# Kernel tuning notes

Measured on AMD Instinct MI355X. Metric: run time of the kernel, lower is better.

Reference implementation:

```python
import jax, jax.numpy as jnp
import numpy as np

D_MODEL = 1024
N_HEADS = 16
D_HIDDEN = 4096
EPS = 1e-6
MASK_VAL = 1e10


def layernorm(x, gamma, beta):
    # Matches torch module: unbiased std (N-1), divide by (std + eps)
    mean = jnp.mean(x, axis=-1, keepdims=True)
    d = x.shape[-1]
    std = jnp.sqrt(jnp.sum((x - mean) ** 2, axis=-1, keepdims=True) / (d - 1))
    return gamma * (x - mean) / (std + EPS) + beta


def multihead(q_in, k_in, v_in, wq, wk, wv, wo, causal):
    # nn.Linear(bias=False): y = x @ W.T
    q = q_in @ wq.T
    k = k_in @ wk.T
    v = v_in @ wv.T
    B, Sq, D = q.shape
    Sk = k.shape[1]
    H, dh = N_HEADS, D // N_HEADS
    q = q.reshape(B, Sq, H, dh)
    k = k.reshape(B, Sk, H, dh)
    v = v.reshape(B, Sk, H, dh)
    scores = jnp.einsum('bqhd,bkhd->bhqk', q, k)  # [B,H,Sq,Sk]
    if causal:
        tri = jnp.triu(jnp.full((Sk, Sk), MASK_VAL, dtype=scores.dtype), k=1)
        scores = scores - tri  # mask applied BEFORE scaling, as in source
    scale = jnp.sqrt(jnp.asarray(D_MODEL, dtype=scores.dtype))  # d_key = d_model
    att = jax.nn.softmax(scores / scale, axis=-1)
    out = jnp.einsum('bhqk,bkhd->bqhd', att, v).reshape(B, Sq, D)
    return out @ wo.T


def setup_inputs() -> dict:
    key = jax.random.key(0)
    ks = jax.random.split(key, 24)
    B, S, D, DH = 2, 2048, D_MODEL, D_HIDDEN
    w = lambda k, shp: (jax.random.normal(k, shp, dtype=jnp.float32) * 0.02)
    inp = {
        'x': jax.random.normal(ks[0], (B, S, D), dtype=jnp.float32),
        'encoding': jax.random.normal(ks[1], (B, S, D), dtype=jnp.float32),
        'sa_wq': w(ks[2], (D, D)), 'sa_wk': w(ks[3], (D, D)),
        'sa_wv': w(ks[4], (D, D)), 'sa_wo': w(ks[5], (D, D)),
        'ca_wq': w(ks[6], (D, D)), 'ca_wk': w(ks[7], (D, D)),
        'ca_wv': w(ks[8], (D, D)), 'ca_wo': w(ks[9], (D, D)),
        'ff_w1': w(ks[10], (DH, D)), 'ff_b1': jnp.zeros((DH,), jnp.float32),
        'ff_w2': w(ks[11], (D, DH)), 'ff_b2': jnp.zeros((D,), jnp.float32),
        'ln1_g': jnp.ones((D,), jnp.float32), 'ln1_b': jnp.zeros((D,), jnp.float32),
        'ln2_g': jnp.ones((D,), jnp.float32), 'ln2_b': jnp.zeros((D,), jnp.float32),
        'ln3_g': jnp.ones((D,), jnp.float32), 'ln3_b': jnp.zeros((D,), jnp.float32),
    }
    return inp


def reference(x, encoding, sa_wq, sa_wk, sa_wv, sa_wo, ca_wq, ca_wk, ca_wv, ca_wo,
              ff_w1, ff_b1, ff_w2, ff_b2, ln1_g, ln1_b, ln2_g, ln2_b, ln3_g, ln3_b):
    # self-attention (causal) + post-norm residual
    h = layernorm(x + multihead(x, x, x, sa_wq, sa_wk, sa_wv, sa_wo, causal=True), ln1_g, ln1_b)
    # cross-attention + post-norm residual
    h = layernorm(h + multihead(h, encoding, encoding, ca_wq, ca_wk, ca_wv, ca_wo, causal=False), ln2_g, ln2_b)
    # feed-forward + post-norm residual
    ff = jax.nn.relu(h @ ff_w1.T + ff_b1) @ ff_w2.T + ff_b2
    return layernorm(h + ff, ln3_g, ln3_b)
```

## Files before the change

kernel.cpp:

```cpp
#include <hip/hip_runtime.h>
#include <hip/hip_bf16.h>
#include <math.h>

#define D_MODEL 1024
#define NHEADS  16
#define DHEAD   64
#define D_HID   4096

typedef __attribute__((ext_vector_type(8))) short short8;
typedef __attribute__((ext_vector_type(4))) short short4v;
typedef __attribute__((ext_vector_type(4))) float f32x4;
typedef __attribute__((ext_vector_type(16))) float f32x16;
typedef __attribute__((ext_vector_type(2))) unsigned uint2v;

#define QSCALE_F 0.04508422002778011f
#define MASK_T   4.5084220e8f

__device__ inline short f2bs(float x) {
    union { __hip_bfloat16 b; short s; } u;
    u.b = __float2bfloat16(x);
    return u.s;
}
__device__ inline float bs2f(ushort s) {
    union { unsigned u; float f; } v; v.u = ((unsigned)s) << 16; return v.f;
}
__device__ inline unsigned cvtpk(float lo, float hi) {
    unsigned r;
    asm("v_cvt_pk_bf16_f32 %0, %1, %2" : "=v"(r) : "v"(lo), "v"(hi));
    return r;
}
__device__ inline short8 pack8(float4 x, float4 y) {
    short8 v;
    v[0] = f2bs(x.x); v[1] = f2bs(x.y); v[2] = f2bs(x.z); v[3] = f2bs(x.w);
    v[4] = f2bs(y.x); v[5] = f2bs(y.y); v[6] = f2bs(y.z); v[7] = f2bs(y.w);
    return v;
}
typedef const unsigned __attribute__((address_space(1))) gu32;
typedef unsigned __attribute__((address_space(3))) lu32;
__device__ inline void gload16(const void* g, void* l) {
    __builtin_amdgcn_global_load_lds((gu32*)g, (lu32*)l, 16, 0, 0);
}
__device__ inline int swz(int r, int byteInRow) {
    return (r * 128 + byteInRow) ^ ((r & 7) << 4);
}

struct WP { const float* p[10]; };
__global__ __launch_bounds__(256) void cast_weights(WP wp, short* __restrict__ dst) {
    const int n8 = (16 << 20) / 8;
    for (int i = blockIdx.x * 256 + threadIdx.x; i < n8; i += gridDim.x * 256) {
        size_t e = (size_t)i * 8;
        int seg = (int)(e >> 20);
        const float* src;
        if (seg < 8)       src = wp.p[seg] + (e & ((1u << 20) - 1));
        else if (seg < 12) src = wp.p[8] + (e - ((size_t)8 << 20));
        else               src = wp.p[9] + (e - ((size_t)12 << 20));
        float4 a = *(const float4*)src;
        float4 b = *(const float4*)(src + 4);
        *(short8*)(dst + e) = pack8(a, b);
    }
}

__global__ __launch_bounds__(256) void cast_f2b(const float* __restrict__ in,
                                                short* __restrict__ out, int n8) {
    for (int i = blockIdx.x * 256 + threadIdx.x; i < n8; i += gridDim.x * 256) {
        float4 a = *(const float4*)(in + (size_t)i * 8);
        float4 b = *(const float4*)(in + (size_t)i * 8 + 4);
        *(short8*)(out + (size_t)i * 8) = pack8(a, b);
    }
}

template<int OM, bool BIAS, bool RELU, bool ACCUM>
__global__ __launch_bounds__(512) void gemm_mfma(
    const short* __restrict__ A, int lda,
    const short* __restrict__ Bm, int ldb,
    const float* __restrict__ bias,
    float* __restrict__ Cf, short* __restrict__ Cb, int ldc,
    int M, int N, int K, size_t routeElems, float qscale)
{
    __shared__ short Als[2][128 * 64];
    __shared__ short Bls[2][128 * 64];

    const int tid = threadIdx.x, w = tid >> 6, l = tid & 63;
    const int l15 = l & 15, lhi = l >> 4;
    const int wr = w >> 2, wc = w & 3;

    const int kh = (OM == 3) ? blockIdx.z : 0;
    if (OM == 3) {
        A  += (size_t)kh * K;
        Bm += (size_t)kh * K;
    }

    const unsigned nwg  = gridDim.x * gridDim.y;
    const unsigned wgid = blockIdx.y * gridDim.x + blockIdx.x;
    const unsigned cpx  = nwg >> 3;
    const unsigned sid  = (wgid & 7) * cpx + (wgid >> 3);
    const int bm = (int)(sid / gridDim.x) * 128;
    const int bn = (int)(sid % gridDim.x) * 128;

    const int srow = w * 8 + (l >> 3);
    const int schk = ((l & 7) ^ (l >> 3)) * 8;

    f32x4 acc[4][2] = {};

    #pragma unroll
    for (int i = 0; i < 2; ++i) {
        const short* ga = A  + (size_t)(bm + i * 64 + srow) * lda + schk;
        const short* gb = Bm + (size_t)(bn + i * 64 + srow) * ldb + schk;
        gload16(ga, &Als[0][i * 4096 + w * 512 + l * 8]);
        gload16(gb, &Bls[0][i * 4096 + w * 512 + l * 8]);
    }
    __syncthreads();

    const int nIter = K >> 6;
    int cur = 0;
    for (int it = 0; it < nIter; ++it) {
        if (it + 1 < nIter) {
            const int k1 = (it + 1) << 6;
            #pragma unroll
            for (int i = 0; i < 2; ++i) {
                const short* ga = A  + (size_t)(bm + i * 64 + srow) * lda + k1 + schk;
                const short* gb = Bm + (size_t)(bn + i * 64 + srow) * ldb + k1 + schk;
                gload16(ga, &Als[cur ^ 1][i * 4096 + w * 512 + l * 8]);
                gload16(gb, &Bls[cur ^ 1][i * 4096 + w * 512 + l * 8]);
            }
        }

        short8 af[4][2], bf[2][2];
        #pragma unroll
        for (int m = 0; m < 4; ++m) {
            const int row = wr * 64 + m * 16 + l15;
            #pragma unroll
            for (int kk = 0; kk < 2; ++kk)
                af[m][kk] = *(const short8*)&Als[cur][row * 64 + (((kk * 4 + lhi) ^ (l15 & 7)) * 8)];
        }
        #pragma unroll
        for (int n = 0; n < 2; ++n) {
            const int row = wc * 32 + n * 16 + l15;
            #pragma unroll
            for (int kk = 0; kk < 2; ++kk)
                bf[n][kk] = *(const short8*)&Bls[cur][row * 64 + (((kk * 4 + lhi) ^ (l15 & 7)) * 8)];
        }
        __builtin_amdgcn_s_setprio(1);
        #pragma unroll
        for (int kk = 0; kk < 2; ++kk)
            #pragma unroll
            for (int m = 0; m < 4; ++m)
                #pragma unroll
                for (int n = 0; n < 2; ++n)
                    acc[m][n] = __builtin_amdgcn_mfma_f32_16x16x32_bf16(af[m][kk], bf[n][kk], acc[m][n], 0, 0, 0);
        __builtin_amdgcn_s_setprio(0);

        __syncthreads();
        cur ^= 1;
    }

    #pragma unroll
    for (int n = 0; n < 2; ++n) {
        const int col = bn + wc * 32 + n * 16 + l15;
        float bv = 0.f;
        if (BIAS && (OM != 3 || kh == 0)) bv = bias[col];
        const float sc = (OM == 2) ? (col < 1024 ? qscale : 1.f) : qscale;
        #pragma unroll
        for (int m = 0; m < 4; ++m) {
            const int row0 = bm + wr * 64 + m * 16 + lhi * 4;
            #pragma unroll
            for (int i = 0; i < 4; ++i) {
                float v = acc[m][n][i] + bv;
                if (ACCUM) v += Cf[(size_t)(row0 + i) * ldc + col];
                if (RELU)  v = fmaxf(v, 0.f);
                v *= sc;
                if (OM == 0) {
                    Cf[(size_t)(row0 + i) * ldc + col] = v;
                } else if (OM == 1) {
                    Cb[(size_t)(row0 + i) * ldc + col] = f2bs(v);
                } else if (OM == 2) {
                    Cb[(size_t)(col >> 10) * routeElems +
                       (size_t)(row0 + i) * 1024 + (col & 1023)] = f2bs(v);
                } else {
                    if (kh == 0) Cf[(size_t)(row0 + i) * ldc + col] = v;
                    else         Cb[(size_t)(row0 + i) * ldc + col] = f2bs(v);
                }
            }
        }
    }
}

__global__ __launch_bounds__(256) void v_prep(
    const short* __restrict__ Vb_, short* __restrict__ Vt, int S)
{
    const int t = blockIdx.x, bh = blockIdx.y;
    const int b = bh >> 4, h = bh & 15;
    const int tid = threadIdx.x;
    const int r = tid >> 2, g = tid & 3;
    __shared__ ushort vs[64][65];

    const size_t inrow = ((size_t)b * S + t * 64 + r) * D_MODEL + h * DHEAD;
    const size_t tbase = ((size_t)bh * (S / 64) + t) * 4096;

    short8 v0 = *(const short8*)(Vb_ + inrow + g * 16);
    short8 v1 = *(const short8*)(Vb_ + inrow + g * 16 + 8);
    #pragma unroll
    for (int j = 0; j < 8; ++j) { vs[r][g * 16 + j] = (ushort)v0[j]; vs[r][g * 16 + 8 + j] = (ushort)v1[j]; }
    __syncthreads();
    short8 q0, q1;
    #pragma unroll
    for (int j = 0; j < 8; ++j) {
        q0[j] = (short)vs[g * 16 + j][r];
        q1[j] = (short)vs[g * 16 + 8 + j][r];
    }
    *(short8*)(Vt + tbase + r * 64 + g * 16)     = q0;
    *(short8*)(Vt + tbase + r * 64 + g * 16 + 8) = q1;
}

template<bool CAUSAL>
__global__ __launch_bounds__(256, 2) void attn_v16(
    const short* __restrict__ Qb, const short* __restrict__ Kr,
    const short* __restrict__ Vt, short* __restrict__ Out, int S)
{
    __shared__ __align__(16) char smem[2 * 32768];

    const int tid = threadIdx.x, w = tid >> 6, l = tid & 63;
    const int l31 = l & 31, hi = l >> 5;

    const unsigned wgid = blockIdx.x;
    int bnd, bh;
    if (CAUSAL) {
        if (wgid < 256) { bh = (int)(wgid & 31); bnd = 15 - (int)(wgid >> 5); }
        else            { unsigned i = wgid - 256; bh = (int)(i & 31); bnd = (int)(i >> 5); }
    } else {
        const unsigned sid = (wgid & 7) * 64 + (wgid >> 3);
        bnd = (int)(sid & 15);
        bh  = (int)(sid >> 4);
    }
    const int b = bh >> 4, h = bh & 15;
    const int qw = bnd * 128 + w * 32;
    const int q  = qw + l31;

    const short* qp = Qb + ((size_t)(b * S + q)) * 1024 + h * 64 + hi * 8;
    short8 bq[4];
    #pragma unroll
    for (int dc = 0; dc < 4; ++dc) bq[dc] = *(const short8*)(qp + dc * 16);

    const short* kbase = Kr + ((size_t)b * S) * 1024 + h * 64;
    const short* vbase = Vt + (size_t)bh * ((S / 64) * 4096);

    f32x16 ot0 = {}, ot1 = {};
    float l_lane = 0.f;

    const int tMax = CAUSAL ? bnd : (S / 128 - 1);

    const int sro  = w * 32 + (l >> 3);
    const int schk = ((l & 7) ^ (l >> 3)) * 8;

    {
        char* Kls = smem;  char* Vls = smem + 16384;
        #pragma unroll
        for (int g = 0; g < 4; ++g) {
            gload16(kbase + (size_t)(sro + g * 8) * 1024 + schk, Kls + (size_t)w * 4096 + g * 1024);
            gload16(vbase + (size_t)(sro + g * 8) * 64   + schk, Vls + (size_t)w * 4096 + g * 1024);
        }
    }
    __syncthreads();

    int cur = 0;
    for (int t = 0; t <= tMax; ++t) {
        if (t + 1 <= tMax) {
            char* Kn = smem + (cur ^ 1) * 32768;
            char* Vn = Kn + 16384;
            #pragma unroll
            for (int g = 0; g < 4; ++g) {
                gload16(kbase + (size_t)((t + 1) * 128 + sro + g * 8) * 1024 + schk, Kn + (size_t)w * 4096 + g * 1024);
                gload16(vbase + (size_t)(t + 1) * 8192 + (size_t)(sro + g * 8) * 64 + schk, Vn + (size_t)w * 4096 + g * 1024);
            }
        }

        const char* Kls = smem + cur * 32768;
        const char* Vls = Kls + 16384;

        #pragma unroll
        for (int sp = 0; sp < 2; ++sp) {
            const int kv0p = t * 128 + sp * 64;
            if (CAUSAL && kv0p > qw + 31) break;

            f32x16 st0 = {}, st1 = {};
            __builtin_amdgcn_s_setprio(1);
            #pragma unroll
            for (int dc = 0; dc < 4; ++dc) {
                short8 a0 = *(const short8*)(Kls + swz(sp * 64 + l31,      dc * 32 + hi * 16));
                short8 a1 = *(const short8*)(Kls + swz(sp * 64 + 32 + l31, dc * 32 + hi * 16));
                st0 = __builtin_amdgcn_mfma_f32_32x32x16_bf16(a0, bq[dc], st0, 0, 0, 0);
                st1 = __builtin_amdgcn_mfma_f32_32x32x16_bf16(a1, bq[dc], st1, 0, 0, 0);
            }
            __builtin_amdgcn_s_setprio(0);

            if (CAUSAL && kv0p + 31 > qw) {
                #pragma unroll
                for (int r = 0; r < 16; ++r) {
                    int kv = kv0p + (r & 3) + 8 * (r >> 2) + 4 * hi;
                    if (kv > q) st0[r] -= MASK_T;
                }
            }
            if (CAUSAL && kv0p + 63 > qw) {
                #pragma unroll
                for (int r = 0; r < 16; ++r) {
                    int kv = kv0p + 32 + (r & 3) + 8 * (r >> 2) + 4 * hi;
                    if (kv > q) st1[r] -= MASK_T;
                }
            }

            union U { unsigned u[4]; short8 s; };
            U c00, c01, c10, c11;
            {
                float p[16];
                #pragma unroll
                for (int r = 0; r < 16; ++r) { p[r] = __builtin_amdgcn_exp2f(st0[r]); l_lane += p[r]; }
                unsigned wd[8];
                #pragma unroll
                for (int i = 0; i < 8; ++i) wd[i] = cvtpk(p[2 * i], p[2 * i + 1]);
                uint2v r0 = __builtin_amdgcn_permlane32_swap(wd[0], wd[2], false, false);
                uint2v r1 = __builtin_amdgcn_permlane32_swap(wd[1], wd[3], false, false);
                uint2v r2 = __builtin_amdgcn_permlane32_swap(wd[4], wd[6], false, false);
                uint2v r3 = __builtin_amdgcn_permlane32_swap(wd[5], wd[7], false, false);
                c00.u[0] = r0[0]; c00.u[2] = r0[1];
                c00.u[1] = r1[0]; c00.u[3] = r1[1];
                c01.u[0] = r2[0]; c01.u[2] = r2[1];
                c01.u[1] = r3[0]; c01.u[3] = r3[1];
            }
            {
                float p[16];
                #pragma unroll
                for (int r = 0; r < 16; ++r) { p[r] = __builtin_amdgcn_exp2f(st1[r]); l_lane += p[r]; }
                unsigned wd[8];
                #pragma unroll
                for (int i = 0; i < 8; ++i) wd[i] = cvtpk(p[2 * i], p[2 * i + 1]);
                uint2v r0 = __builtin_amdgcn_permlane32_swap(wd[0], wd[2], false, false);
                uint2v r1 = __builtin_amdgcn_permlane32_swap(wd[1], wd[3], false, false);
                uint2v r2 = __builtin_amdgcn_permlane32_swap(wd[4], wd[6], false, false);
                uint2v r3 = __builtin_amdgcn_permlane32_swap(wd[5], wd[7], false, false);
                c10.u[0] = r0[0]; c10.u[2] = r0[1];
                c10.u[1] = r1[0]; c10.u[3] = r1[1];
                c11.u[0] = r2[0]; c11.u[2] = r2[1];
                c11.u[1] = r3[0]; c11.u[3] = r3[1];
            }

            const char* Vsp = Vls + sp * 8192;
            __builtin_amdgcn_s_setprio(1);
            short8 av;
            av  = *(const short8*)(Vsp + swz(l31,      hi * 16));
            ot0 = __builtin_amdgcn_mfma_f32_32x32x16_bf16(av, c00.s, ot0, 0, 0, 0);
            av  = *(const short8*)(Vsp + swz(32 + l31, hi * 16));
            ot1 = __builtin_amdgcn_mfma_f32_32x32x16_bf16(av, c00.s, ot1, 0, 0, 0);
            av  = *(const short8*)(Vsp + swz(l31,      32 + hi * 16));
            ot0 = __builtin_amdgcn_mfma_f32_32x32x16_bf16(av, c01.s, ot0, 0, 0, 0);
            av  = *(const short8*)(Vsp + swz(32 + l31, 32 + hi * 16));
            ot1 = __builtin_amdgcn_mfma_f32_32x32x16_bf16(av, c01.s, ot1, 0, 0, 0);
            av  = *(const short8*)(Vsp + swz(l31,      64 + hi * 16));
            ot0 = __builtin_amdgcn_mfma_f32_32x32x16_bf16(av, c10.s, ot0, 0, 0, 0);
            av  = *(const short8*)(Vsp + swz(32 + l31, 64 + hi * 16));
            ot1 = __builtin_amdgcn_mfma_f32_32x32x16_bf16(av, c10.s, ot1, 0, 0, 0);
            av  = *(const short8*)(Vsp + swz(l31,      96 + hi * 16));
            ot0 = __builtin_amdgcn_mfma_f32_32x32x16_bf16(av, c11.s, ot0, 0, 0, 0);
            av  = *(const short8*)(Vsp + swz(32 + l31, 96 + hi * 16));
            ot1 = __builtin_amdgcn_mfma_f32_32x32x16_bf16(av, c11.s, ot1, 0, 0, 0);
            __builtin_amdgcn_s_setprio(0);
        }

        __syncthreads();
        cur ^= 1;
    }

    const float l_tot = l_lane + __shfl_xor(l_lane, 32, 64);
    const float inv = 1.f / l_tot;
    short* orow = Out + ((size_t)(b * S + q)) * 1024 + h * 64;
    #pragma unroll
    for (int i = 0; i < 8; ++i) {
        int dbase = ((2 * i) & 3) + 8 * (i >> 1) + 4 * hi;
        *(unsigned*)(orow + dbase)      = cvtpk(ot0[2 * i] * inv, ot0[2 * i + 1] * inv);
        *(unsigned*)(orow + 32 + dbase) = cvtpk(ot1[2 * i] * inv, ot1[2 * i + 1] * inv);
    }
}

template<bool IN1BF, bool OUTBF, bool P3>
__global__ __launch_bounds__(256) void add_ln(
    const void* __restrict__ in1, const float* __restrict__ in2,
    const short* __restrict__ in3,
    const float* __restrict__ gam, const float* __restrict__ bet,
    void* __restrict__ y)
{
    const int row = blockIdx.x;
    const int tid = threadIdx.x;
    const size_t off = (size_t)row * D_MODEL;

    float a0, a1, a2, a3;
    if (IN1BF) {
        short4v xs = ((const short4v*)((const short*)in1 + off))[tid];
        a0 = bs2f((ushort)xs[0]); a1 = bs2f((ushort)xs[1]);
        a2 = bs2f((ushort)xs[2]); a3 = bs2f((ushort)xs[3]);
    } else {
        float4 xv = ((const float4*)((const float*)in1 + off))[tid];
        a0 = xv.x; a1 = xv.y; a2 = xv.z; a3 = xv.w;
    }
    float4 rv = ((const float4*)(in2 + off))[tid];
    float v0 = a0 + rv.x, v1 = a1 + rv.y, v2 = a2 + rv.z, v3 = a3 + rv.w;
    if (P3) {
        short4v ps = ((const short4v*)(in3 + off))[tid];
        v0 += bs2f((ushort)ps[0]); v1 += bs2f((ushort)ps[1]);
        v2 += bs2f((ushort)ps[2]); v3 += bs2f((ushort)ps[3]);
    }

    float s  = v0 + v1 + v2 + v3;
    float ss = v0 * v0 + v1 * v1 + v2 * v2 + v3 * v3;

    __shared__ float sb[8];
    #pragma unroll
    for (int o = 32; o > 0; o >>= 1) {
        s  += __shfl_down(s, o, 64);
        ss += __shfl_down(ss, o, 64);
    }
    const int lane = tid & 63, w = tid >> 6;
    if (lane == 0) { sb[w] = s; sb[4 + w] = ss; }
    __syncthreads();
    float S  = sb[0] + sb[1] + sb[2] + sb[3];
    float SS = sb[4] + sb[5] + sb[6] + sb[7];

    float mean = S * (1.f / D_MODEL);
    float var_sum = SS - S * mean;
    float stdv = sqrtf(var_sum * (1.f / (D_MODEL - 1)));
    float inv = 1.f / (stdv + 1e-6f);

    float4 gv = ((const float4*)gam)[tid];
    float4 bv = ((const float4*)bet)[tid];
    float o0 = gv.x * (v0 - mean) * inv + bv.x;
    float o1 = gv.y * (v1 - mean) * inv + bv.y;
    float o2 = gv.z * (v2 - mean) * inv + bv.z;
    float o3 = gv.w * (v3 - mean) * inv + bv.w;
    if (OUTBF) {
        short4v ov; ov[0] = f2bs(o0); ov[1] = f2bs(o1); ov[2] = f2bs(o2); ov[3] = f2bs(o3);
        ((short4v*)((short*)y + off))[tid] = ov;
    } else {
        ((float4*)((float*)y + off))[tid] = make_float4(o0, o1, o2, o3);
    }
}

extern "C" void kernel_launch(void* const* d_in, const int* in_sizes, int n_in,
                              void* d_out, int out_size, void* d_ws, size_t ws_size,
                              hipStream_t stream)
{
    const float* x     = (const float*)d_in[0];
    const float* enc   = (const float*)d_in[1];
    WP wp;
    for (int i = 0; i < 8; ++i) wp.p[i] = (const float*)d_in[2 + i];
    wp.p[8] = (const float*)d_in[10];
    wp.p[9] = (const float*)d_in[12];
    const float* ff_b1 = (const float*)d_in[11];
    const float* ff_b2 = (const float*)d_in[13];
    const float* ln1_g = (const float*)d_in[14];
    const float* ln1_b = (const float*)d_in[15];
    const float* ln2_g = (const float*)d_in[16];
    const float* ln2_b = (const float*)d_in[17];
    const float* ln3_g = (const float*)d_in[18];
    const float* ln3_b = (const float*)d_in[19];
    float* out = (float*)d_out;

    const int Bn = 2, S = 2048, M = Bn * S;
    const size_t MB = 1u << 20;
    char* ws = (char*)d_ws;
    short* Wb   = (short*)(ws);
    short* p32  = (short*)(ws + 32 * MB);
    short* p40  = (short*)(ws + 40 * MB);
    short* p48  = (short*)(ws + 48 * MB);
    short* p56  = (short*)(ws + 56 * MB);
    short* p64  = (short*)(ws + 64 * MB);
    short* p72  = (short*)(ws + 72 * MB);
    float* f0   = (float*)(ws + 80 * MB);

    short* tbuf = p48;

    const size_t RT = 4 * MB;
    const short* W_saqkv = Wb;
    const short* W_sawo  = Wb + 3 * MB;
    const short* W_caq   = Wb + 4 * MB;
    const short* W_cakv  = Wb + 5 * MB;
    const short* W_cawo  = Wb + 7 * MB;
    const short* W_ff1   = Wb + 8 * MB;
    const short* W_ff2   = Wb + 12 * MB;

    dim3 blk(256);
    dim3 blk512(512);
    dim3 g_qkv(3072 / 128, M / 128);
    dim3 g_kv(2048 / 128, M / 128);
    dim3 g_n1k(1024 / 128, M / 128);
    dim3 g_spl(1024 / 128, M / 128, 2);
    dim3 g_ff1(4096 / 128, M / 128);
    dim3 g_attn(512);
    dim3 g_vp(S / 64, Bn * NHEADS);
    dim3 g_ln(M);

    cast_weights<<<2048, blk, 0, stream>>>(wp, Wb);
    cast_f2b<<<2048, blk, 0, stream>>>(x, p32, (M * D_MODEL) / 8);
    cast_f2b<<<2048, blk, 0, stream>>>(enc, p64, (M * D_MODEL) / 8);

    gemm_mfma<2,false,false,false><<<g_qkv, blk512, 0, stream>>>(p32, 1024, W_saqkv, 1024, nullptr, nullptr, p40, 1024, M, 3072, 1024, RT, QSCALE_F);
    v_prep<<<g_vp, blk, 0, stream>>>(p56, p72, S);
    attn_v16<true><<<g_attn, blk, 0, stream>>>(p40, p48, p72, p32, S);
    gemm_mfma<3,false,false,false><<<g_spl, blk512, 0, stream>>>(p32, 1024, W_sawo, 1024, nullptr, f0, p48, 1024, M, 1024, 512, 0, 1.f);
    add_ln<false,true,true><<<g_ln, blk, 0, stream>>>(x, f0, p48, ln1_g, ln1_b, p32);

    gemm_mfma<2,false,false,false><<<g_kv, blk512, 0, stream>>>(p64, 1024, W_cakv, 1024, nullptr, nullptr, p48, 1024, M, 2048, 1024, RT, 1.f);
    gemm_mfma<1,false,false,false><<<g_n1k, blk512, 0, stream>>>(p32, 1024, W_caq, 1024, nullptr, nullptr, p40, 1024, M, 1024, 1024, 0, QSCALE_F);
    v_prep<<<g_vp, blk, 0, stream>>>(p56, p72, S);
    attn_v16<false><<<g_attn, blk, 0, stream>>>(p40, p48, p72, p56, S);
    gemm_mfma<3,false,false,false><<<g_spl, blk512, 0, stream>>>(p56, 1024, W_cawo, 1024, nullptr, f0, p48, 1024, M, 1024, 512, 0, 1.f);
    add_ln<true,true,true><<<g_ln, blk, 0, stream>>>(p32, f0, p48, ln2_g, ln2_b, p40);

    gemm_mfma<1,true,true,false><<<g_ff1, blk512, 0, stream>>>(p40, 1024, W_ff1, 1024, ff_b1, nullptr, tbuf, 4096, M, 4096, 1024, 0, 1.f);
    gemm_mfma<3,true,false,false><<<g_spl, blk512, 0, stream>>>(tbuf, 4096, W_ff2, 4096, ff_b2, f0, p32, 1024, M, 1024, 2048, 0, 1.f);
    add_ln<true,false,true><<<g_ln, blk, 0, stream>>>(p40, f0, p32, ln3_g, ln3_b, out);
}
```

Baseline: 323.0 us.

## Fuse V transpose into QKV GEMM epilogue and split softmax row-sum accumulators

The QKV and cross-attention KV projection GEMMs now write the V segment straight into the tiled, transposed layout that attention expects, using short4 stores, and the two v_prep launches are removed. This saves a kernel launch and a full read/write pass over V for each attention. In exchange the V epilogue stores are strided rather than row-contiguous. The softmax row sum is also split into four independent partial accumulators to shorten the serial add chain.

Result: no change. 317.8 us (-1.6%).

```diff
diff --git a/kernel.cpp b/kernel.cpp
--- a/kernel.cpp
+++ b/kernel.cpp
@@ -75,7 +75,7 @@
     const short* __restrict__ Bm, int ldb,
     const float* __restrict__ bias,
     float* __restrict__ Cf, short* __restrict__ Cb, int ldc,
-    int M, int N, int K, size_t routeElems, float qscale)
+    int M, int N, int K, size_t routeElems, float qscale, int vseg)
 {
     __shared__ short Als[2][128 * 64];
     __shared__ short Bls[2][128 * 64];
@@ -163,6 +163,18 @@
         #pragma unroll
         for (int m = 0; m < 4; ++m) {
             const int row0 = bm + wr * 64 + m * 16 + lhi * 4;
+            if (OM == 2 && (col >> 10) == vseg) {
+                const int s = row0 & 2047, bb = row0 >> 11;
+                const int vcol = col & 1023;
+                short* vt = (short*)Cf;
+                const size_t dst = ((size_t)((bb * 16 + (vcol >> 6)) * 32 + (s >> 6))) * 4096
+                                 + (size_t)(vcol & 63) * 64 + (s & 63);
+                short4v sv;
+                #pragma unroll
+                for (int i = 0; i < 4; ++i) sv[i] = f2bs(acc[m][n][i]);
+                *(short4v*)(vt + dst) = sv;
+                continue;
+            }
             #pragma unroll
             for (int i = 0; i < 4; ++i) {
                 float v = acc[m][n][i] + bv;
@@ -185,35 +197,8 @@
     }
 }
 
-__global__ __launch_bounds__(256) void v_prep(
-    const short* __restrict__ Vb_, short* __restrict__ Vt, int S)
-{
-    const int t = blockIdx.x, bh = blockIdx.y;
-    const int b = bh >> 4, h = bh & 15;
-    const int tid = threadIdx.x;
-    const int r = tid >> 2, g = tid & 3;
-    __shared__ ushort vs[64][65];
-
-    const size_t inrow = ((size_t)b * S + t * 64 + r) * D_MODEL + h * DHEAD;
-    const size_t tbase = ((size_t)bh * (S / 64) + t) * 4096;
-
-    short8 v0 = *(const short8*)(Vb_ + inrow + g * 16);
-    short8 v1 = *(const short8*)(Vb_ + inrow + g * 16 + 8);
-    #pragma unroll
-    for (int j = 0; j < 8; ++j) { vs[r][g * 16 + j] = (ushort)v0[j]; vs[r][g * 16 + 8 + j] = (ushort)v1[j]; }
-    __syncthreads();
-    short8 q0, q1;
-    #pragma unroll
-    for (int j = 0; j < 8; ++j) {
-        q0[j] = (short)vs[g * 16 + j][r];
-        q1[j] = (short)vs[g * 16 + 8 + j][r];
-    }
-    *(short8*)(Vt + tbase + r * 64 + g * 16)     = q0;
-    *(short8*)(Vt + tbase + r * 64 + g * 16 + 8) = q1;
-}
-
 template<bool CAUSAL>
-__global__ __launch_bounds__(256, 2) void attn_v16(
+__global__ __launch_bounds__(256, 2) void attn_v17(
     const short* __restrict__ Qb, const short* __restrict__ Kr,
     const short* __restrict__ Vt, short* __restrict__ Out, int S)
 {
@@ -313,7 +298,11 @@
             {
                 float p[16];
                 #pragma unroll
-                for (int r = 0; r < 16; ++r) { p[r] = __builtin_amdgcn_exp2f(st0[r]); l_lane += p[r]; }
+                for (int r = 0; r < 16; ++r) p[r] = __builtin_amdgcn_exp2f(st0[r]);
+                float u0 = 0.f, u1 = 0.f, u2 = 0.f, u3 = 0.f;
+                #pragma unroll
+                for (int r = 0; r < 16; r += 4) { u0 += p[r]; u1 += p[r + 1]; u2 += p[r + 2]; u3 += p[r + 3]; }
+                l_lane += (u0 + u1) + (u2 + u3);
                 unsigned wd[8];
                 #pragma unroll
                 for (int i = 0; i < 8; ++i) wd[i] = cvtpk(p[2 * i], p[2 * i + 1]);
@@ -329,7 +318,11 @@
             {
                 float p[16];
                 #pragma unroll
-                for (int r = 0; r < 16; ++r) { p[r] = __builtin_amdgcn_exp2f(st1[r]); l_lane += p[r]; }
+                for (int r = 0; r < 16; ++r) p[r] = __builtin_amdgcn_exp2f(st1[r]);
+                float u0 = 0.f, u1 = 0.f, u2 = 0.f, u3 = 0.f;
+                #pragma unroll
+                for (int r = 0; r < 16; r += 4) { u0 += p[r]; u1 += p[r + 1]; u2 += p[r + 2]; u3 += p[r + 3]; }
+                l_lane += (u0 + u1) + (u2 + u3);
                 unsigned wd[8];
                 #pragma unroll
                 for (int i = 0; i < 8; ++i) wd[i] = cvtpk(p[2 * i], p[2 * i + 1]);
@@ -493,27 +486,24 @@
     dim3 g_spl(1024 / 128, M / 128, 2);
     dim3 g_ff1(4096 / 128, M / 128);
     dim3 g_attn(512);
-    dim3 g_vp(S / 64, Bn * NHEADS);
     dim3 g_ln(M);
 
     cast_weights<<<2048, blk, 0, stream>>>(wp, Wb);
     cast_f2b<<<2048, blk, 0, stream>>>(x, p32, (M * D_MODEL) / 8);
     cast_f2b<<<2048, blk, 0, stream>>>(enc, p64, (M * D_MODEL) / 8);
 
-    gemm_mfma<2,false,false,false><<<g_qkv, blk512, 0, stream>>>(p32, 1024, W_saqkv, 1024, nullptr, nullptr, p40, 1024, M, 3072, 1024, RT, QSCALE_F);
-    v_prep<<<g_vp, blk, 0, stream>>>(p56, p72, S);
-    attn_v16<true><<<g_attn, blk, 0, stream>>>(p40, p48, p72, p32, S);
-    gemm_mfma<3,false,false,false><<<g_spl, blk512, 0, stream>>>(p32, 1024, W_sawo, 1024, nullptr, f0, p48, 1024, M, 1024, 512, 0, 1.f);
+    gemm_mfma<2,false,false,false><<<g_qkv, blk512, 0, stream>>>(p32, 1024, W_saqkv, 1024, nullptr, (float*)p72, p40, 1024, M, 3072, 1024, RT, QSCALE_F, 2);
+    attn_v17<true><<<g_attn, blk, 0, stream>>>(p40, p48, p72, p32, S);
+    gemm_mfma<3,false,false,false><<<g_spl, blk512, 0, stream>>>(p32, 1024, W_sawo, 1024, nullptr, f0, p48, 1024, M, 1024, 512, 0, 1.f, 99);
     add_ln<false,true,true><<<g_ln, blk, 0, stream>>>(x, f0, p48, ln1_g, ln1_b, p32);
 
-    gemm_mfma<2,false,false,false><<<g_kv, blk512, 0, stream>>>(p64, 1024, W_cakv, 1024, nullptr, nullptr, p48, 1024, M, 2048, 1024, RT, 1.f);
-    gemm_mfma<1,false,false,false><<<g_n1k, blk512, 0, stream>>>(p32, 1024, W_caq, 1024, nullptr, nullptr, p40, 1024, M, 1024, 1024, 0, QSCALE_F);
-    v_prep<<<g_vp, blk, 0, stream>>>(p56, p72, S);
-    attn_v16<false><<<g_attn, blk, 0, stream>>>(p40, p48, p72, p56, S);
-    gemm_mfma<3,false,false,false><<<g_spl, blk512, 0, stream>>>(p56, 1024, W_cawo, 1024, nullptr, f0, p48, 1024, M, 1024, 512, 0, 1.f);
+    gemm_mfma<2,false,false,false><<<g_kv, blk512, 0, stream>>>(p64, 1024, W_cakv, 1024, nullptr, (float*)p72, p48, 1024, M, 2048, 1024, RT, 1.f, 1);
+    gemm_mfma<1,false,false,false><<<g_n1k, blk512, 0, stream>>>(p32, 1024, W_caq, 1024, nullptr, nullptr, p40, 1024, M, 1024, 1024, 0, QSCALE_F, 99);
+    attn_v17<false><<<g_attn, blk, 0, stream>>>(p40, p48, p72, p56, S);
+    gemm_mfma<3,false,false,false><<<g_spl, blk512, 0, stream>>>(p56, 1024, W_cawo, 1024, nullptr, f0, p48, 1024, M, 1024, 512, 0, 1.f, 99);
     add_ln<true,true,true><<<g_ln, blk, 0, stream>>>(p32, f0, p48, ln2_g, ln2_b, p40);
 
-    gemm_mfma<1,true,true,false><<<g_ff1, blk512, 0, stream>>>(p40, 1024, W_ff1, 1024, ff_b1, nullptr, tbuf, 4096, M, 4096, 1024, 0, 1.f);
-    gemm_mfma<3,true,false,false><<<g_spl, blk512, 0, stream>>>(tbuf, 4096, W_ff2, 4096, ff_b2, f0, p32, 1024, M, 1024, 2048, 0, 1.f);
+    gemm_mfma<1,true,true,false><<<g_ff1, blk512, 0, stream>>>(p40, 1024, W_ff1, 1024, ff_b1, nullptr, tbuf, 4096, M, 4096, 1024, 0, 1.f, 99);
+    gemm_mfma<3,true,false,false><<<g_spl, blk512, 0, stream>>>(tbuf, 4096, W_ff2, 4096, ff_b2, f0, p32, 1024, M, 1024, 2048, 0, 1.f, 99);
     add_ln<true,false,true><<<g_ln, blk, 0, stream>>>(p40, f0, p32, ln3_g, ln3_b, out);
 }
```
